# Optimization experiments

Measured on AMD Instinct MI355X. Metric: run time of the kernel, lower is better.

The kernel has to match this reference:

```python
import jax, jax.numpy as jnp
import numpy as np

D_MODEL = 768
D_INNER = 1536      # d_model * expand
D_STATE = 128
D_CONV = 4
HEADDIM = 64
NHEADS = 24         # d_inner / headdim
CONV_DIM = D_INNER + 2 * D_STATE          # 1792
D_IN_PROJ = 2 * D_INNER + 2 * D_STATE + NHEADS  # 3352
EPS = 1e-5
BATCH, SEQLEN = 4, 2048


def setup_inputs() -> dict:
    key = jax.random.key(0)
    ks = jax.random.split(key, 8)
    u = jax.random.normal(ks[0], (BATCH, SEQLEN, D_MODEL), dtype=jnp.float32)
    W_in = jax.random.normal(ks[1], (D_IN_PROJ, D_MODEL), dtype=jnp.float32) * 0.02
    conv_w = jax.random.normal(ks[2], (CONV_DIM, D_CONV), dtype=jnp.float32) * 0.2
    conv_b = jnp.zeros((CONV_DIM,), dtype=jnp.float32)
    # dt_bias = inverse-softplus of dt sampled log-uniformly in [dt_min, dt_max]
    dt = jnp.exp(jax.random.uniform(ks[3], (NHEADS,)) * (np.log(0.1) - np.log(0.001)) + np.log(0.001))
    dt = jnp.clip(dt, 1e-4, None)
    dt_bias = dt + jnp.log(-jnp.expm1(-dt))
    A_log = jnp.log(jax.random.uniform(ks[4], (NHEADS,), minval=1.0, maxval=16.0))
    D = jnp.ones((NHEADS,), dtype=jnp.float32)
    norm_w = jnp.ones((D_INNER,), dtype=jnp.float32)
    W_out = jax.random.normal(ks[5], (D_MODEL, D_INNER), dtype=jnp.float32) * 0.02
    return {"u": u, "W_in": W_in, "conv_w": conv_w, "conv_b": conv_b,
            "dt_bias": dt_bias, "A_log": A_log, "D": D, "norm_w": norm_w, "W_out": W_out}


def reference(u, W_in, conv_w, conv_b, dt_bias, A_log, D, norm_w, W_out):
    b, L, _ = u.shape
    zxbcdt = jnp.einsum('bld,ed->ble', u, W_in)  # (b, L, 3352)
    z = zxbcdt[..., :D_INNER]
    xBC = zxbcdt[..., D_INNER:D_INNER + CONV_DIM]
    dt = zxbcdt[..., D_INNER + CONV_DIM:]        # (b, L, nheads)

    # causal depthwise conv1d (kernel width 4), then SiLU
    xp = jnp.pad(xBC, ((0, 0), (D_CONV - 1, 0), (0, 0)))
    xBC = sum(xp[:, k:k + L, :] * conv_w[:, k] for k in range(D_CONV)) + conv_b
    xBC = jax.nn.silu(xBC)

    x = xBC[..., :D_INNER].reshape(b, L, NHEADS, HEADDIM)
    B = xBC[..., D_INNER:D_INNER + D_STATE]      # (b, L, n)  (ngroups=1)
    C = xBC[..., D_INNER + D_STATE:]             # (b, L, n)

    dt = jax.nn.softplus(dt + dt_bias)           # (b, L, h)
    A = -jnp.exp(A_log)                          # (h,)
    dA = jnp.exp(dt * A)                         # (b, L, h)

    def step(h, inp):
        dA_t, dt_t, x_t, B_t, C_t = inp
        # h: (b, h, p, n)
        h = h * dA_t[:, :, None, None] + jnp.einsum('bhp,bh,bn->bhpn', x_t, dt_t, B_t)
        y = jnp.einsum('bhpn,bn->bhp', h, C_t)
        return h, y

    xs = (jnp.swapaxes(dA, 0, 1), jnp.swapaxes(dt, 0, 1), jnp.swapaxes(x, 0, 1),
          jnp.swapaxes(B, 0, 1), jnp.swapaxes(C, 0, 1))
    h0 = jnp.zeros((b, NHEADS, HEADDIM, D_STATE), dtype=u.dtype)
    _, ys = jax.lax.scan(step, h0, xs)           # ys: (L, b, h, p)
    y = jnp.swapaxes(ys, 0, 1)                   # (b, L, h, p)

    y = y + D[None, None, :, None] * x           # skip connection
    y = y.reshape(b, L, D_INNER)

    # RMSNorm then gate with silu(z)
    y = norm_w * y * jax.lax.rsqrt(jnp.mean(y * y, axis=-1, keepdims=True) + EPS)
    y = y * jax.nn.silu(z)
    return jnp.einsum('bld,ed->ble', y, W_out)
```

## Files before the change

kernel.cpp:

```cpp
#include <hip/hip_runtime.h>
#include <hip/hip_bf16.h>

typedef __bf16 bf16x8 __attribute__((ext_vector_type(8)));
typedef float f32x4 __attribute__((ext_vector_type(4)));
typedef unsigned int u32x4 __attribute__((ext_vector_type(4)));

#define MTOT    8192
#define DMODEL  768
#define DINNER  1536
#define DSTATE  128
#define NHEADS  24
#define CONVDIM 1792
#define LDZ     3328
#define SEQ     2048
#define CHUNK   128
#define NCHUNK  16
#define NBH     96

#define NU   (MTOT*DMODEL)
#define NWI  (LDZ*DMODEL)
#define NWO  (DMODEL*DINNER)
#define NWD  (32*DMODEL)

__device__ __forceinline__ void gl2lds16(const __hip_bfloat16* g, __hip_bfloat16* l) {
  __builtin_amdgcn_global_load_lds((const __attribute__((address_space(1))) void*)g,
                                   (__attribute__((address_space(3))) void*)l, 16, 0, 0);
}

__global__ __launch_bounds__(256) void cvt_bf16(const float* __restrict__ u, const float* __restrict__ Wi,
                                                const float* __restrict__ Wo,
                                                __hip_bfloat16* __restrict__ ub, __hip_bfloat16* __restrict__ wib,
                                                __hip_bfloat16* __restrict__ wob,
                                                __hip_bfloat16* __restrict__ wdh, __hip_bfloat16* __restrict__ wdl) {
  int i = blockIdx.x * 256 + threadIdx.x;
  if (i < NU) ub[i] = __float2bfloat16(u[i]);
  else if (i < NU + NWI) { int k = i - NU; wib[k] = __float2bfloat16(Wi[k]); }
  else if (i < NU + NWI + NWO) { int k = i - NU - NWI; wob[k] = __float2bfloat16(Wo[k]); }
  else if (i < NU + NWI + NWO + 2 * NWD) {
    int k = i - NU - NWI - NWO;
    int lo = (k >= NWD);
    if (lo) k -= NWD;
    int row = k / DMODEL, col = k - row * DMODEL;
    float w = (row < NHEADS) ? Wi[(size_t)(LDZ + row) * DMODEL + col] : 0.f;
    __hip_bfloat16 h = __float2bfloat16(w);
    if (!lo) wdh[k] = h;
    else wdl[k] = __float2bfloat16(w - __bfloat162float(h));
  }
}

#define STG_R(s)                                                                               \
  {                                                                                            \
    const int sl_ = (s) & 3;                                                                   \
    _Pragma("unroll") for (int i_ = 0; i_ < CA; ++i_)                                          \
        gl2lds16(Ag + (size_t)(i_ * RA) * lda + (s) * 32, &As[sl_][i_ * (T * 8) + tid * 8]);   \
    _Pragma("unroll") for (int i_ = 0; i_ < CB; ++i_)                                          \
        gl2lds16(Bg + (size_t)(i_ * RA) * ldb + (s) * 32, &Bs[sl_][i_ * (T * 8) + tid * 8]);   \
  }

#define PHASE_R(t, DOSTG, VMW)                                                                 \
  {                                                                                            \
    if (DOSTG) STG_R((t) + 3);                                                                 \
    const int sl_ = (t) & 3;                                                                   \
    bf16x8 fa_[FM], fb_[FN];                                                                   \
    _Pragma("unroll") for (int i_ = 0; i_ < FM; ++i_)                                          \
        fa_[i_] = *(const bf16x8*)&As[sl_][(wm * PM + i_ * 16 + lr) * 32 + rch];               \
    _Pragma("unroll") for (int j_ = 0; j_ < FN; ++j_)                                          \
        fb_[j_] = *(const bf16x8*)&Bs[sl_][(wn * PN + j_ * 16 + lr) * 32 + rch];               \
    __builtin_amdgcn_s_setprio(1);                                                             \
    _Pragma("unroll") for (int i_ = 0; i_ < FM; ++i_)                                          \
        _Pragma("unroll") for (int j_ = 0; j_ < FN; ++j_)                                      \
            acc[i_][j_] =                                                                      \
                __builtin_amdgcn_mfma_f32_16x16x32_bf16(fa_[i_], fb_[j_], acc[i_][j_], 0, 0, 0); \
    __builtin_amdgcn_s_setprio(0);                                                             \
    VMW;                                                                                       \
    __builtin_amdgcn_sched_barrier(0);                                                         \
    __builtin_amdgcn_s_barrier();                                                              \
    __builtin_amdgcn_sched_barrier(0);                                                         \
  }

template <int BM, int BN, int WGM, int WGN, typename OutT>
__global__ __launch_bounds__(WGM * WGN * 64, 2) void gemm_ring(const __hip_bfloat16* __restrict__ A,
                                                               const __hip_bfloat16* __restrict__ B,
                                                               OutT* __restrict__ C, int lda, int ldb,
                                                               int ldc, int nsub, int nbn) {
  constexpr int T = WGM * WGN * 64;
  constexpr int PM = BM / WGM, PN = BN / WGN;
  constexpr int FM = PM / 16, FN = PN / 16;
  constexpr int CA = (BM * 64) / (T * 16);
  constexpr int CB = (BN * 64) / (T * 16);
  constexpr int RA = T / 4;
  __shared__ __align__(16) __hip_bfloat16 As[4][BM * 32];
  __shared__ __align__(16) __hip_bfloat16 Bs[4][BN * 32];
  const int tid = threadIdx.x;
  const int lane = tid & 63, wid = tid >> 6;
  const int wm = wid / WGN, wn = wid % WGN;
  const int lr = lane & 15, lk = lane >> 4;
  const int cpx = (int)gridDim.x >> 3;
  const int swz = ((int)blockIdx.x & 7) * cpx + ((int)blockIdx.x >> 3);
  const int bn = swz % nbn, bm = swz / nbn;
  const int srow = tid >> 2;
  const int scol = ((tid & 3) ^ ((tid >> 3) & 3)) * 8;
  const __hip_bfloat16* Ag = A + (size_t)(bm * BM + srow) * lda + scol;
  const __hip_bfloat16* Bg = B + (size_t)(bn * BN + srow) * ldb + scol;
  const int rch = (lk ^ ((lr >> 1) & 3)) * 8;
  f32x4 acc[FM][FN] = {};

  STG_R(0); STG_R(1); STG_R(2);
  asm volatile("s_waitcnt vmcnt(8)" ::: "memory");
  __builtin_amdgcn_sched_barrier(0);
  __builtin_amdgcn_s_barrier();
  __builtin_amdgcn_sched_barrier(0);
  int t = 0;
  for (; t < nsub - 3; ++t) PHASE_R(t, true, asm volatile("s_waitcnt vmcnt(8)" ::: "memory"));
  PHASE_R(t, false, asm volatile("s_waitcnt vmcnt(4)" ::: "memory")); ++t;
  PHASE_R(t, false, asm volatile("s_waitcnt vmcnt(0)" ::: "memory")); ++t;
  PHASE_R(t, false, (void)0);

  const int crow0 = bm * BM + wm * PM + lk * 4;
  const int ccol0 = bn * BN + wn * PN + lr;
#pragma unroll
  for (int mf = 0; mf < FM; ++mf)
#pragma unroll
    for (int nf = 0; nf < FN; ++nf)
#pragma unroll
      for (int r = 0; r < 4; ++r)
        C[(size_t)(crow0 + mf * 16 + r) * ldc + ccol0 + nf * 16] = (OutT)acc[mf][nf][r];
}

__global__ __launch_bounds__(256) void dt_mfma(const float* __restrict__ u,
                                               const __hip_bfloat16* __restrict__ wdh,
                                               const __hip_bfloat16* __restrict__ wdl,
                                               const float* __restrict__ dtb, const float* __restrict__ alog,
                                               float* __restrict__ dtS, float* __restrict__ dtA) {
  __shared__ __align__(16) __hip_bfloat16 Uh[64 * 32];
  __shared__ __align__(16) __hip_bfloat16 Ul[64 * 32];
  const int tid = threadIdx.x;
  const int lane = tid & 63, wid = tid >> 6;
  const int lr = lane & 15, lk = lane >> 4;
  const int bm = blockIdx.x;
  const int r = tid >> 2, c0 = (tid & 3) * 8;
  const float* usrc = u + (size_t)(bm * 64 + r) * DMODEL + c0;
  f32x4 acc[2] = {};
  for (int ks = 0; ks < DMODEL / 32; ++ks) {
    float4 v0 = *(const float4*)(usrc + ks * 32);
    float4 v1 = *(const float4*)(usrc + ks * 32 + 4);
    bf16x8 hi, lo;
    const float* vf = (const float*)&v0;
#pragma unroll
    for (int e = 0; e < 4; ++e) {
      __hip_bfloat16 h = __float2bfloat16(vf[e]);
      hi[e] = *(__bf16*)&h;
      __hip_bfloat16 l2 = __float2bfloat16(vf[e] - __bfloat162float(h));
      lo[e] = *(__bf16*)&l2;
    }
    vf = (const float*)&v1;
#pragma unroll
    for (int e = 0; e < 4; ++e) {
      __hip_bfloat16 h = __float2bfloat16(vf[e]);
      hi[4 + e] = *(__bf16*)&h;
      __hip_bfloat16 l2 = __float2bfloat16(vf[e] - __bfloat162float(h));
      lo[4 + e] = *(__bf16*)&l2;
    }
    *(bf16x8*)&Uh[r * 32 + c0] = hi;
    *(bf16x8*)&Ul[r * 32 + c0] = lo;
    __syncthreads();
    bf16x8 ah = *(const bf16x8*)&Uh[(wid * 16 + lr) * 32 + lk * 8];
    bf16x8 al = *(const bf16x8*)&Ul[(wid * 16 + lr) * 32 + lk * 8];
#pragma unroll
    for (int j = 0; j < 2; ++j) {
      bf16x8 bh = *(const bf16x8*)(wdh + (size_t)(j * 16 + lr) * DMODEL + ks * 32 + lk * 8);
      bf16x8 bl = *(const bf16x8*)(wdl + (size_t)(j * 16 + lr) * DMODEL + ks * 32 + lk * 8);
      acc[j] = __builtin_amdgcn_mfma_f32_16x16x32_bf16(ah, bh, acc[j], 0, 0, 0);
      acc[j] = __builtin_amdgcn_mfma_f32_16x16x32_bf16(ah, bl, acc[j], 0, 0, 0);
      acc[j] = __builtin_amdgcn_mfma_f32_16x16x32_bf16(al, bh, acc[j], 0, 0, 0);
    }
    __syncthreads();
  }
#pragma unroll
  for (int j = 0; j < 2; ++j) {
    int col = j * 16 + lr;
    if (col < NHEADS) {
      float nA = -expf(alog[col]);
      float bia = dtb[col];
#pragma unroll
      for (int rr = 0; rr < 4; ++rr) {
        int row = bm * 64 + wid * 16 + lk * 4 + rr;
        float x = acc[j][rr] + bia;
        float dt = (x > 20.f) ? x : log1pf(expf(x));
        dtS[(size_t)row * NHEADS + col] = dt;
        dtA[(size_t)row * NHEADS + col] = nA * dt;
      }
    }
  }
}

__global__ __launch_bounds__(256) void cumsum_kernel(const float* __restrict__ dtA, float* __restrict__ scum,
                                                     float* __restrict__ cdec) {
  int bc = blockIdx.x;
  int b = bc >> 4, c = bc & 15;
  __shared__ float buf[CHUNK * NHEADS];
  int m0 = b * SEQ + c * CHUNK;
  for (int t = threadIdx.x; t < CHUNK * NHEADS; t += 256)
    buf[t] = dtA[(size_t)m0 * NHEADS + t];
  __syncthreads();
  if (threadIdx.x < NHEADS) {
    int h = threadIdx.x;
    float run = 0.f;
    float* dst = scum + ((size_t)bc * NHEADS + h) * CHUNK;
    for (int j = 0; j < CHUNK; ++j) { run += buf[j * NHEADS + h]; dst[j] = run; }
    cdec[(b * NHEADS + h) * NCHUNK + c] = __expf(run);
  }
}

__global__ __launch_bounds__(256) void conv_fused(const __hip_bfloat16* __restrict__ zxb,
                                                  const float* __restrict__ cw,
                                                  const float* __restrict__ cb, const float* __restrict__ dtS,
                                                  __hip_bfloat16* __restrict__ Xd, __hip_bfloat16* __restrict__ Bb,
                                                  __hip_bfloat16* __restrict__ Cb, __hip_bfloat16* __restrict__ XdT,
                                                  __hip_bfloat16* __restrict__ Bt) {
  __shared__ __hip_bfloat16 t[64][72];
  __shared__ float dts_sh[64];
  const int c0 = blockIdx.x * 64, m0 = blockIdx.y * 64;
  const int b = m0 >> 11, l0 = m0 & (SEQ - 1);
  const int tid = threadIdx.x;
  const int c = tid & 63, rg = tid >> 6;
  const int gc = c0 + c;
  const bool isX = (c0 < DINNER);
  if (isX && tid < 64) dts_sh[tid] = dtS[(size_t)(m0 + tid) * NHEADS + (c0 >> 6)];
  const float4 w = *(const float4*)(cw + (size_t)gc * 4);
  const float bias = cb[gc];
  const __hip_bfloat16* src = zxb + (size_t)(m0 + rg * 16) * LDZ + DINNER + gc;
  const int lbase = l0 + rg * 16;
  float v0 = (lbase >= 3) ? __bfloat162float(src[-3 * (ptrdiff_t)LDZ]) : 0.f;
  float v1 = (lbase >= 2) ? __bfloat162float(src[-2 * (ptrdiff_t)LDZ]) : 0.f;
  float v2 = (lbase >= 1) ? __bfloat162float(src[-1 * (ptrdiff_t)LDZ]) : 0.f;
  __syncthreads();
#pragma unroll
  for (int r = 0; r < 16; ++r) {
    float v3 = __bfloat162float(src[(ptrdiff_t)r * LDZ]);
    float a = bias + v0 * w.x + v1 * w.y + v2 * w.z + v3 * w.w;
    float sv = a / (1.f + __expf(-a));
    int lm = rg * 16 + r;
    __hip_bfloat16 val = __float2bfloat16(isX ? dts_sh[lm] * sv : sv);
    t[lm][c] = val;
    int m = m0 + lm;
    if (isX) Xd[(size_t)m * DINNER + gc] = val;
    else if (gc < DINNER + DSTATE) Bb[(size_t)m * DSTATE + gc - DINNER] = val;
    else Cb[(size_t)m * DSTATE + gc - DINNER - DSTATE] = val;
    v0 = v1; v1 = v2; v2 = v3;
  }
  __syncthreads();
  if (c0 < DINNER + DSTATE) {
    int r2 = tid >> 2, cc = (tid & 3) * 16;
    __hip_bfloat16 tmp[16] __attribute__((aligned(16)));
#pragma unroll
    for (int k = 0; k < 16; ++k) tmp[k] = t[cc + k][r2];
    __hip_bfloat16* dst = isX ? XdT + ((size_t)(b * DINNER + c0 + r2)) * SEQ + l0 + cc
                              : Bt + ((size_t)(b * DSTATE + (c0 - DINNER) + r2)) * SEQ + l0 + cc;
    *(u32x4*)dst = *(u32x4*)&tmp[0];
    *(u32x4*)(dst + 8) = *(u32x4*)&tmp[8];
  }
}

__global__ __launch_bounds__(256, 2) void state_gemm(const __hip_bfloat16* __restrict__ XdT,
                                                     const __hip_bfloat16* __restrict__ Bt,
                                                     const float* __restrict__ scum,
                                                     __hip_bfloat16* __restrict__ cstat) {
  __shared__ __align__(16) __hip_bfloat16 Xw[64 * 136];
  __shared__ __align__(16) __hip_bfloat16 Bts[128 * 136];
  __shared__ float rS[CHUNK];
  int bid = blockIdx.x;
  int c = bid & 15, bh = bid >> 4;
  int b = bh / NHEADS, h = bh % NHEADS;
  const float* sp = scum + ((size_t)(b * NCHUNK + c) * NHEADS + h) * CHUNK;
  int tid = threadIdx.x;
  if (tid < CHUNK) rS[tid] = __expf(sp[CHUNK - 1] - sp[tid]);
  {
    int n = tid >> 1, jc = (tid & 1) * 64;
    const __hip_bfloat16* g = Bt + ((size_t)(b * DSTATE + n)) * SEQ + c * CHUNK + jc;
#pragma unroll
    for (int q = 0; q < 8; ++q) *(u32x4*)&Bts[n * 136 + jc + q * 8] = *(const u32x4*)(g + q * 8);
  }
  __syncthreads();
  {
    int p = tid >> 2, jc = (tid & 3) * 32;
    const __hip_bfloat16* g = XdT + ((size_t)((b * NHEADS + h) * 64 + p)) * SEQ + c * CHUNK + jc;
#pragma unroll
    for (int q = 0; q < 4; ++q) {
      bf16x8 vv = *(const bf16x8*)(g + q * 8);
      bf16x8 ov;
#pragma unroll
      for (int e = 0; e < 8; ++e) ov[e] = (__bf16)((float)vv[e] * rS[jc + q * 8 + e]);
      *(bf16x8*)&Xw[p * 136 + jc + q * 8] = ov;
    }
  }
  __syncthreads();
  const int lane = tid & 63, wid = tid >> 6;
  const int wm = wid >> 1, wn = wid & 1;
  const int lr = lane & 15, lk = lane >> 4;
  f32x4 acc[2][4] = {};
#pragma unroll
  for (int ks = 0; ks < 4; ++ks) {
    bf16x8 af[2], bq[4];
#pragma unroll
    for (int i = 0; i < 2; ++i) af[i] = *(const bf16x8*)&Xw[(wm * 32 + i * 16 + lr) * 136 + ks * 32 + lk * 8];
#pragma unroll
    for (int j = 0; j < 4; ++j) bq[j] = *(const bf16x8*)&Bts[(wn * 64 + j * 16 + lr) * 136 + ks * 32 + lk * 8];
#pragma unroll
    for (int i = 0; i < 2; ++i)
#pragma unroll
      for (int j = 0; j < 4; ++j)
        acc[i][j] = __builtin_amdgcn_mfma_f32_16x16x32_bf16(af[i], bq[j], acc[i][j], 0, 0, 0);
  }
  __hip_bfloat16* dst = cstat + (size_t)bid * 8192;
#pragma unroll
  for (int i = 0; i < 2; ++i)
#pragma unroll
    for (int j = 0; j < 4; ++j)
#pragma unroll
      for (int r = 0; r < 4; ++r)
        dst[(wm * 32 + i * 16 + lk * 4 + r) * 128 + wn * 64 + j * 16 + lr] = __float2bfloat16(acc[i][j][r]);
}

__global__ __launch_bounds__(256) void scanB(__hip_bfloat16* __restrict__ cstat, const float* __restrict__ cdec) {
  const int bh = blockIdx.x >> 3, sl = blockIdx.x & 7;
  const int base = sl * 1024 + threadIdx.x * 4;
  float hreg[4] = {0.f, 0.f, 0.f, 0.f};
  for (int c = 0; c < NCHUNK; ++c) {
    __hip_bfloat16* p = cstat + (size_t)(bh * NCHUNK + c) * 8192 + base;
    const float P = cdec[bh * NCHUNK + c];
    __hip_bfloat16 tmp[4], hs[4];
    *(uint2*)tmp = *(const uint2*)p;
#pragma unroll
    for (int j = 0; j < 4; ++j) hs[j] = __float2bfloat16(hreg[j]);
    *(uint2*)p = *(uint2*)hs;
#pragma unroll
    for (int j = 0; j < 4; ++j) hreg[j] = fmaf(hreg[j], P, __bfloat162float(tmp[j]));
  }
}

template <int JE>
__global__ __launch_bounds__(256, 2) void ssd_y(const __hip_bfloat16* __restrict__ Cb,
                                                const __hip_bfloat16* __restrict__ Bb,
                                                const __hip_bfloat16* __restrict__ XdT,
                                                const __hip_bfloat16* __restrict__ Xd,
                                                const __hip_bfloat16* __restrict__ cstat,
                                                const float* __restrict__ scum,
                                                const float* __restrict__ dtS, const float* __restrict__ Dvec,
                                                __hip_bfloat16* __restrict__ zxb) {
  constexpr int HI = JE - 64;
  constexpr int JW = JE / 2;
  constexpr int FJ = JW / 16;
  constexpr int KJ = JE / 32;
  __shared__ __align__(16) __hip_bfloat16 Cs[64 * 136];
  __shared__ __align__(16) __hip_bfloat16 Bs[JE * 136];
  __shared__ __align__(16) __hip_bfloat16 R3[64 * 136];
  __shared__ float sS[CHUNK];
  int bid = blockIdx.x;
  int c = bid & 15, bh = bid >> 4;
  int b = bh / NHEADS, h = bh % NHEADS;
  int m0 = b * SEQ + c * CHUNK;
  int tid = threadIdx.x;
  const float* sp = scum + ((size_t)(b * NCHUNK + c) * NHEADS + h) * CHUNK;
  if (tid < CHUNK) sS[tid] = sp[tid];
  {
    int r = tid >> 2, nc = (tid & 3) * 32;
    const __hip_bfloat16* g = Cb + (size_t)(m0 + HI + r) * DSTATE + nc;
#pragma unroll
    for (int q = 0; q < 4; ++q) *(u32x4*)&Cs[r * 136 + nc + q * 8] = *(const u32x4*)(g + q * 8);
  }
  if (JE == 64) {
    int r = tid >> 2, nc = (tid & 3) * 32;
    const __hip_bfloat16* g = Bb + (size_t)(m0 + r) * DSTATE + nc;
#pragma unroll
    for (int q = 0; q < 4; ++q) *(u32x4*)&Bs[r * 136 + nc + q * 8] = *(const u32x4*)(g + q * 8);
  } else {
    int r = tid >> 1, nc = (tid & 1) * 64;
    const __hip_bfloat16* g = Bb + (size_t)(m0 + r) * DSTATE + nc;
#pragma unroll
    for (int q = 0; q < 8; ++q) *(u32x4*)&Bs[r * 136 + nc + q * 8] = *(const u32x4*)(g + q * 8);
  }
  {
    int p = tid >> 2, nc = (tid & 3) * 32;
    const __hip_bfloat16* g = cstat + (size_t)bid * 8192 + p * 128 + nc;
#pragma unroll
    for (int q = 0; q < 4; ++q) *(u32x4*)&R3[p * 136 + nc + q * 8] = *(const u32x4*)(g + q * 8);
  }
  __syncthreads();
  const int lane = tid & 63, wid = tid >> 6;
  const int wm = wid >> 1, wn = wid & 1;
  const int lr = lane & 15, lk = lane >> 4;
  f32x4 Gacc[2][FJ] = {};
  f32x4 Uacc[2][2] = {};
#pragma unroll
  for (int ks = 0; ks < 4; ++ks) {
    bf16x8 af[2], bq[2];
#pragma unroll
    for (int i = 0; i < 2; ++i) af[i] = *(const bf16x8*)&Cs[(wm * 32 + i * 16 + lr) * 136 + ks * 32 + lk * 8];
#pragma unroll
    for (int j = 0; j < 2; ++j) bq[j] = *(const bf16x8*)&R3[(wn * 32 + j * 16 + lr) * 136 + ks * 32 + lk * 8];
#pragma unroll
    for (int i = 0; i < 2; ++i)
#pragma unroll
      for (int j = 0; j < 2; ++j)
        Uacc[i][j] = __builtin_amdgcn_mfma_f32_16x16x32_bf16(af[i], bq[j], Uacc[i][j], 0, 0, 0);
  }
#pragma unroll
  for (int ks = 0; ks < 4; ++ks) {
    bf16x8 af[2], bq[FJ];
#pragma unroll
    for (int i = 0; i < 2; ++i) af[i] = *(const bf16x8*)&Cs[(wm * 32 + i * 16 + lr) * 136 + ks * 32 + lk * 8];
#pragma unroll
    for (int j = 0; j < FJ; ++j) bq[j] = *(const bf16x8*)&Bs[(wn * JW + j * 16 + lr) * 136 + ks * 32 + lk * 8];
#pragma unroll
    for (int i = 0; i < 2; ++i)
#pragma unroll
      for (int j = 0; j < FJ; ++j)
        Gacc[i][j] = __builtin_amdgcn_mfma_f32_16x16x32_bf16(af[i], bq[j], Gacc[i][j], 0, 0, 0);
  }
  __syncthreads();
  {
    float siv[2][4];
#pragma unroll
    for (int i = 0; i < 2; ++i)
#pragma unroll
      for (int r = 0; r < 4; ++r) siv[i][r] = sS[HI + wm * 32 + i * 16 + lk * 4 + r];
#pragma unroll
    for (int i = 0; i < 2; ++i)
#pragma unroll
      for (int j = 0; j < FJ; ++j) {
        int gj = wn * JW + j * 16 + lr;
        float sj = sS[gj];
#pragma unroll
        for (int r = 0; r < 4; ++r) {
          int il = wm * 32 + i * 16 + lk * 4 + r;
          int gi = HI + il;
          float mv = (gj <= gi) ? Gacc[i][j][r] * __expf(siv[i][r] - sj) : 0.f;
          Cs[il * 136 + gj] = __float2bfloat16(mv);
        }
      }
  }
  {
    int p = tid >> 2, jc = (tid & 3) * (JE / 4);
    const __hip_bfloat16* g = XdT + ((size_t)((b * NHEADS + h) * 64 + p)) * SEQ + c * CHUNK + jc;
#pragma unroll
    for (int q = 0; q < JE / 32; ++q) *(u32x4*)&R3[p * 136 + jc + q * 8] = *(const u32x4*)(g + q * 8);
  }
  __syncthreads();
  f32x4 Yacc[2][2] = {};
#pragma unroll
  for (int ks = 0; ks < KJ; ++ks) {
    bf16x8 af[2], bq[2];
#pragma unroll
    for (int i = 0; i < 2; ++i) af[i] = *(const bf16x8*)&Cs[(wm * 32 + i * 16 + lr) * 136 + ks * 32 + lk * 8];
#pragma unroll
    for (int j = 0; j < 2; ++j) bq[j] = *(const bf16x8*)&R3[(wn * 32 + j * 16 + lr) * 136 + ks * 32 + lk * 8];
#pragma unroll
    for (int i = 0; i < 2; ++i)
#pragma unroll
      for (int j = 0; j < 2; ++j)
        Yacc[i][j] = __builtin_amdgcn_mfma_f32_16x16x32_bf16(af[i], bq[j], Yacc[i][j], 0, 0, 0);
  }
  const float Dh = Dvec[h];
#pragma unroll
  for (int i = 0; i < 2; ++i)
#pragma unroll
    for (int r = 0; r < 4; ++r) {
      int il = wm * 32 + i * 16 + lk * 4 + r;
      int gi = HI + il;
      int m = m0 + gi;
      float ei = __expf(sS[gi]);
      float dt = dtS[(size_t)m * NHEADS + h];
#pragma unroll
      for (int j = 0; j < 2; ++j) {
        int p = wn * 32 + j * 16 + lr;
        float xv = (float)Xd[(size_t)m * DINNER + h * 64 + p] / dt;
        zxb[(size_t)m * LDZ + DINNER + h * 64 + p] =
            __float2bfloat16(Yacc[i][j][r] + ei * Uacc[i][j][r] + Dh * xv);
      }
    }
}

__global__ __launch_bounds__(192) void norm_gate(const __hip_bfloat16* __restrict__ zxb,
                                                 const float* __restrict__ nw,
                                                 __hip_bfloat16* __restrict__ yg) {
  const int m = blockIdx.x, tid = threadIdx.x;
  const __hip_bfloat16* zr = zxb + (size_t)m * LDZ;
  const __hip_bfloat16* yr = zr + DINNER;
  bf16x8 y8 = *(const bf16x8*)&yr[tid * 8];
  bf16x8 z8 = *(const bf16x8*)&zr[tid * 8];
  float yv[8], zv[8];
  float ss = 0.f;
#pragma unroll
  for (int e = 0; e < 8; ++e) {
    yv[e] = (float)y8[e];
    zv[e] = (float)z8[e];
    ss = fmaf(yv[e], yv[e], ss);
  }
#pragma unroll
  for (int o = 32; o > 0; o >>= 1) ss += __shfl_down(ss, o);
  __shared__ float red[3];
  if ((tid & 63) == 0) red[tid >> 6] = ss;
  __syncthreads();
  float tot = red[0] + red[1] + red[2];
  float r = rsqrtf(tot * (1.f / 1536.f) + 1e-5f);
  float4 w0 = *(const float4*)&nw[tid * 8];
  float4 w1 = *(const float4*)&nw[tid * 8 + 4];
  const float* wf = (const float*)&w0;
  bf16x8 o8;
#pragma unroll
  for (int e = 0; e < 8; ++e) {
    float wv = (e < 4) ? wf[e] : ((const float*)&w1)[e - 4];
    float g = zv[e] / (1.f + __expf(-zv[e]));
    o8[e] = (__bf16)(wv * yv[e] * r * g);
  }
  *(bf16x8*)&yg[(size_t)m * DINNER + tid * 8] = o8;
}

extern "C" void kernel_launch(void* const* d_in, const int* in_sizes, int n_in,
                              void* d_out, int out_size, void* d_ws, size_t ws_size,
                              hipStream_t stream) {
  (void)in_sizes; (void)n_in; (void)out_size; (void)ws_size;
  const float* u       = (const float*)d_in[0];
  const float* W_in    = (const float*)d_in[1];
  const float* conv_w  = (const float*)d_in[2];
  const float* conv_b  = (const float*)d_in[3];
  const float* dt_bias = (const float*)d_in[4];
  const float* A_log   = (const float*)d_in[5];
  const float* Dvec    = (const float*)d_in[6];
  const float* norm_w  = (const float*)d_in[7];
  const float* W_out   = (const float*)d_in[8];
  float* out = (float*)d_out;

  __hip_bfloat16* zxbb = (__hip_bfloat16*)d_ws;
  __hip_bfloat16* cstatb = zxbb + (size_t)MTOT * LDZ;
  float* dtS  = (float*)(cstatb + (size_t)NBH * NCHUNK * 8192);
  float* dtA  = dtS + (size_t)MTOT * NHEADS;
  float* scum = dtA + (size_t)MTOT * NHEADS;
  float* cdec = scum + (size_t)MTOT * NHEADS;
  __hip_bfloat16* ub  = (__hip_bfloat16*)(cdec + NBH * NCHUNK);
  __hip_bfloat16* wib = ub + (size_t)NU;
  __hip_bfloat16* wob = wib + (size_t)NWI;
  __hip_bfloat16* wdh = wob + (size_t)NWO;
  __hip_bfloat16* wdl = wdh + (size_t)NWD;
  __hip_bfloat16* Xd  = wdl + (size_t)NWD;
  __hip_bfloat16* Bb  = Xd + (size_t)MTOT * DINNER;
  __hip_bfloat16* Cb  = Bb + (size_t)MTOT * DSTATE;
  __hip_bfloat16* XdT = Cb + (size_t)MTOT * DSTATE;
  __hip_bfloat16* Bt  = XdT + (size_t)MTOT * DINNER;
  __hip_bfloat16* yg  = Xd;

  cvt_bf16<<<(NU + NWI + NWO + 2 * NWD + 255) / 256, 256, 0, stream>>>(u, W_in, W_out, ub, wib, wob, wdh, wdl);
  gemm_ring<256, 256, 2, 4, __hip_bfloat16><<<(LDZ / 256) * (MTOT / 256), 512, 0, stream>>>(
      ub, wib, zxbb, DMODEL, DMODEL, LDZ, DMODEL / 32, LDZ / 256);
  dt_mfma<<<MTOT / 64, 256, 0, stream>>>(u, wdh, wdl, dt_bias, A_log, dtS, dtA);
  cumsum_kernel<<<64, 256, 0, stream>>>(dtA, scum, cdec);
  conv_fused<<<dim3(CONVDIM / 64, MTOT / 64), 256, 0, stream>>>(zxbb, conv_w, conv_b, dtS, Xd, Bb, Cb, XdT, Bt);
  state_gemm<<<NBH * NCHUNK, 256, 0, stream>>>(XdT, Bt, scum, cstatb);
  scanB<<<NBH * 8, 256, 0, stream>>>(cstatb, cdec);
  ssd_y<64><<<NBH * NCHUNK, 256, 0, stream>>>(Cb, Bb, XdT, Xd, cstatb, scum, dtS, Dvec, zxbb);
  ssd_y<128><<<NBH * NCHUNK, 256, 0, stream>>>(Cb, Bb, XdT, Xd, cstatb, scum, dtS, Dvec, zxbb);
  norm_gate<<<MTOT, 192, 0, stream>>>(zxbb, norm_w, yg);
  gemm_ring<128, 128, 2, 2, float><<<(DMODEL / 128) * (MTOT / 128), 256, 0, stream>>>(
      yg, wob, out, DINNER, DINNER, DMODEL, DINNER / 32, DMODEL / 128);
}
```

Before: 339.1 us.

## Replace 4-stage GEMM ring with 3-buffer pipeline and split M-half MFMA phases

The bf16 GEMM kernel moves from a 4-slot LDS ring with prefetch distance 3 to a 3-slot ring with prefetch distance 2. For the large in-projection GEMM, each k-step is also split into two M-halves, each with its own barrier, so A-fragment reads interleave with MFMA work. The smaller LDS footprint can improve occupancy. In exchange there are more barriers per k-step and less latency hiding for global loads.

```diff
diff --git a/kernel.cpp b/kernel.cpp
--- a/kernel.cpp
+++ b/kernel.cpp
@@ -48,49 +48,30 @@
   }
 }
 
-#define STG_R(s)                                                                               \
-  {                                                                                            \
-    const int sl_ = (s) & 3;                                                                   \
-    _Pragma("unroll") for (int i_ = 0; i_ < CA; ++i_)                                          \
-        gl2lds16(Ag + (size_t)(i_ * RA) * lda + (s) * 32, &As[sl_][i_ * (T * 8) + tid * 8]);   \
-    _Pragma("unroll") for (int i_ = 0; i_ < CB; ++i_)                                          \
-        gl2lds16(Bg + (size_t)(i_ * RA) * ldb + (s) * 32, &Bs[sl_][i_ * (T * 8) + tid * 8]);   \
-  }
-
-#define PHASE_R(t, DOSTG, VMW)                                                                 \
-  {                                                                                            \
-    if (DOSTG) STG_R((t) + 3);                                                                 \
-    const int sl_ = (t) & 3;                                                                   \
-    bf16x8 fa_[FM], fb_[FN];                                                                   \
-    _Pragma("unroll") for (int i_ = 0; i_ < FM; ++i_)                                          \
-        fa_[i_] = *(const bf16x8*)&As[sl_][(wm * PM + i_ * 16 + lr) * 32 + rch];               \
-    _Pragma("unroll") for (int j_ = 0; j_ < FN; ++j_)                                          \
-        fb_[j_] = *(const bf16x8*)&Bs[sl_][(wn * PN + j_ * 16 + lr) * 32 + rch];               \
-    __builtin_amdgcn_s_setprio(1);                                                             \
-    _Pragma("unroll") for (int i_ = 0; i_ < FM; ++i_)                                          \
-        _Pragma("unroll") for (int j_ = 0; j_ < FN; ++j_)                                      \
-            acc[i_][j_] =                                                                      \
-                __builtin_amdgcn_mfma_f32_16x16x32_bf16(fa_[i_], fb_[j_], acc[i_][j_], 0, 0, 0); \
-    __builtin_amdgcn_s_setprio(0);                                                             \
-    VMW;                                                                                       \
-    __builtin_amdgcn_sched_barrier(0);                                                         \
-    __builtin_amdgcn_s_barrier();                                                              \
-    __builtin_amdgcn_sched_barrier(0);                                                         \
-  }
-
-template <int BM, int BN, int WGM, int WGN, typename OutT>
-__global__ __launch_bounds__(WGM * WGN * 64, 2) void gemm_ring(const __hip_bfloat16* __restrict__ A,
-                                                               const __hip_bfloat16* __restrict__ B,
-                                                               OutT* __restrict__ C, int lda, int ldb,
-                                                               int ldc, int nsub, int nbn) {
+#define STG3(t_)                                                                          \
+  {                                                                                       \
+    __hip_bfloat16* ab_ = As[(t_) % 3];                                                   \
+    __hip_bfloat16* bb_ = Bs[(t_) % 3];                                                   \
+    _Pragma("unroll") for (int i_ = 0; i_ < CA; ++i_)                                     \
+        gl2lds16(Ag + (size_t)(i_ * RPC) * lda + (size_t)(t_) * 32, ab_ + i_ * (T * 8) + ldst); \
+    _Pragma("unroll") for (int i_ = 0; i_ < CB; ++i_)                                     \
+        gl2lds16(Bg + (size_t)(i_ * RPC) * ldb + (size_t)(t_) * 32, bb_ + i_ * (T * 8) + ldst); \
+  }
+
+template <int BM, int BN, int WGM, int WGN, int MH, typename OutT>
+__global__ __launch_bounds__(WGM * WGN * 64, 2) void gemm_r3(const __hip_bfloat16* __restrict__ A,
+                                                             const __hip_bfloat16* __restrict__ B,
+                                                             OutT* __restrict__ C, int lda, int ldb,
+                                                             int ldc, int nt, int nbn) {
   constexpr int T = WGM * WGN * 64;
   constexpr int PM = BM / WGM, PN = BN / WGN;
   constexpr int FM = PM / 16, FN = PN / 16;
-  constexpr int CA = (BM * 64) / (T * 16);
-  constexpr int CB = (BN * 64) / (T * 16);
-  constexpr int RA = T / 4;
-  __shared__ __align__(16) __hip_bfloat16 As[4][BM * 32];
-  __shared__ __align__(16) __hip_bfloat16 Bs[4][BN * 32];
+  constexpr int FMH = FM / MH;
+  constexpr int CA = (BM * 4) / T;
+  constexpr int CB = (BN * 4) / T;
+  constexpr int RPC = T / 4;
+  __shared__ __align__(16) __hip_bfloat16 As[3][BM * 32];
+  __shared__ __align__(16) __hip_bfloat16 Bs[3][BN * 32];
   const int tid = threadIdx.x;
   const int lane = tid & 63, wid = tid >> 6;
   const int wm = wid / WGN, wn = wid % WGN;
@@ -102,20 +83,51 @@
   const int scol = ((tid & 3) ^ ((tid >> 3) & 3)) * 8;
   const __hip_bfloat16* Ag = A + (size_t)(bm * BM + srow) * lda + scol;
   const __hip_bfloat16* Bg = B + (size_t)(bn * BN + srow) * ldb + scol;
-  const int rch = (lk ^ ((lr >> 1) & 3)) * 8;
+  const int ach = (lk ^ ((lr >> 1) & 3)) * 8;
+  const int ldst = wid * 512;
   f32x4 acc[FM][FN] = {};
-
-  STG_R(0); STG_R(1); STG_R(2);
-  asm volatile("s_waitcnt vmcnt(8)" ::: "memory");
+  bf16x8 bF[FN], aF[FMH];
+
+  STG3(0);
+  STG3(1);
+  asm volatile("s_waitcnt vmcnt(4)" ::: "memory");
   __builtin_amdgcn_sched_barrier(0);
   __builtin_amdgcn_s_barrier();
   __builtin_amdgcn_sched_barrier(0);
-  int t = 0;
-  for (; t < nsub - 3; ++t) PHASE_R(t, true, asm volatile("s_waitcnt vmcnt(8)" ::: "memory"));
-  PHASE_R(t, false, asm volatile("s_waitcnt vmcnt(4)" ::: "memory")); ++t;
-  PHASE_R(t, false, asm volatile("s_waitcnt vmcnt(0)" ::: "memory")); ++t;
-  PHASE_R(t, false, (void)0);
-
+  for (int t = 0; t < nt; ++t) {
+    const __hip_bfloat16* ab = As[t % 3];
+    const __hip_bfloat16* bb = Bs[t % 3];
+#pragma unroll
+    for (int p = 0; p < MH; ++p) {
+      if (p == 0) {
+#pragma unroll
+        for (int j = 0; j < FN; ++j)
+          bF[j] = *(const bf16x8*)&bb[(wn * PN + j * 16 + lr) * 32 + ach];
+        if (t + 2 < nt) STG3(t + 2);
+      }
+#pragma unroll
+      for (int i = 0; i < FMH; ++i)
+        aF[i] = *(const bf16x8*)&ab[(wm * PM + (p * FMH + i) * 16 + lr) * 32 + ach];
+      __builtin_amdgcn_sched_barrier(0);
+      __builtin_amdgcn_s_barrier();
+      __builtin_amdgcn_sched_barrier(0);
+      __builtin_amdgcn_s_setprio(1);
+#pragma unroll
+      for (int i = 0; i < FMH; ++i)
+#pragma unroll
+        for (int j = 0; j < FN; ++j)
+          acc[p * FMH + i][j] =
+              __builtin_amdgcn_mfma_f32_16x16x32_bf16(aF[i], bF[j], acc[p * FMH + i][j], 0, 0, 0);
+      __builtin_amdgcn_s_setprio(0);
+      if (p == MH - 1) {
+        if (t + 2 < nt) { asm volatile("s_waitcnt vmcnt(4)" ::: "memory"); }
+        else if (t + 1 < nt) { asm volatile("s_waitcnt vmcnt(0)" ::: "memory"); }
+      }
+      __builtin_amdgcn_sched_barrier(0);
+      __builtin_amdgcn_s_barrier();
+      __builtin_amdgcn_sched_barrier(0);
+    }
+  }
   const int crow0 = bm * BM + wm * PM + lk * 4;
   const int ccol0 = bn * BN + wn * PN + lr;
 #pragma unroll
@@ -551,7 +563,7 @@
   __hip_bfloat16* yg  = Xd;
 
   cvt_bf16<<<(NU + NWI + NWO + 2 * NWD + 255) / 256, 256, 0, stream>>>(u, W_in, W_out, ub, wib, wob, wdh, wdl);
-  gemm_ring<256, 256, 2, 4, __hip_bfloat16><<<(LDZ / 256) * (MTOT / 256), 512, 0, stream>>>(
+  gemm_r3<256, 256, 2, 4, 2, __hip_bfloat16><<<(LDZ / 256) * (MTOT / 256), 512, 0, stream>>>(
       ub, wib, zxbb, DMODEL, DMODEL, LDZ, DMODEL / 32, LDZ / 256);
   dt_mfma<<<MTOT / 64, 256, 0, stream>>>(u, wdh, wdl, dt_bias, A_log, dtS, dtA);
   cumsum_kernel<<<64, 256, 0, stream>>>(dtA, scum, cdec);
@@ -561,6 +573,6 @@
   ssd_y<64><<<NBH * NCHUNK, 256, 0, stream>>>(Cb, Bb, XdT, Xd, cstatb, scum, dtS, Dvec, zxbb);
   ssd_y<128><<<NBH * NCHUNK, 256, 0, stream>>>(Cb, Bb, XdT, Xd, cstatb, scum, dtS, Dvec, zxbb);
   norm_gate<<<MTOT, 192, 0, stream>>>(zxbb, norm_w, yg);
-  gemm_ring<128, 128, 2, 2, float><<<(DMODEL / 128) * (MTOT / 128), 256, 0, stream>>>(
+  gemm_r3<128, 128, 2, 2, 1, float><<<(DMODEL / 128) * (MTOT / 128), 256, 0, stream>>>(
       yg, wob, out, DINNER, DINNER, DMODEL, DINNER / 32, DMODEL / 128);
 }
```

Measured after the change: 354.8 us. 1.05x slower.
